# Performance work log

Measured on AMD Instinct MI355X. Metric: run time of the kernel, lower is better.

The kernel has to match this reference:

```python
import jax, jax.numpy as jnp
import numpy as np

B, T, C, H = 4, 4096, 1024, 64

def setup_inputs() -> dict:
    key = jax.random.key(0)
    k1, k2, k3, k4, k5 = jax.random.split(key, 5)
    scale = 0.02
    return {
        "x": jax.random.normal(k1, (B, T, C), dtype=jnp.float32),
        "head_bias": jax.random.normal(k2, (T, T), dtype=jnp.float32) * 0.1,
        "w_k": jax.random.normal(k3, (C, H), dtype=jnp.float32) * scale,
        "w_q": jax.random.normal(k4, (C, H), dtype=jnp.float32) * scale,
        "w_v": jax.random.normal(k5, (C, H), dtype=jnp.float32) * scale,
    }

def reference(x, head_bias, w_k, w_q, w_v):
    # x: (B,T,C) ; projections: (B,T,H)
    k = jnp.einsum('btc,ch->bth', x, w_k)
    q = jnp.einsum('btc,ch->bth', x, w_q)
    v = jnp.einsum('btc,ch->bth', x, w_v)
    Tq = x.shape[1]
    # scores: (B,T,T) with RPE bias and causal mask
    scores = jnp.einsum('bqh,bkh->bqk', q, k) * (k.shape[-1] ** -0.5)
    scores = scores + head_bias[None, :, :]
    causal = jnp.tril(jnp.ones((Tq, Tq), dtype=bool))
    scores = jnp.where(causal[None, :, :], scores, -jnp.inf)
    weights = jax.nn.softmax(scores, axis=-1)
    out = jnp.einsum('bqk,bkh->bqh', weights, v)
    return out
```

## Files before the change

kernel.cpp:

```cpp
#include <hip/hip_runtime.h>
#include <hip/hip_bf16.h>


#define T_DIM 4096
#define C_DIM 1024
#define KT    64
#define CK    256

typedef __attribute__((ext_vector_type(8))) short s16x8;
typedef __attribute__((ext_vector_type(4))) float f32x4;
typedef __attribute__((ext_vector_type(2))) unsigned int u32x2;

__device__ __forceinline__ short f2bf(float f) {
    unsigned u = __builtin_bit_cast(unsigned, f);
    u += 0x7FFFu + ((u >> 16) & 1u);
    return (short)(u >> 16);
}
__device__ __forceinline__ unsigned pack2(float a, float b) {
    unsigned ua = __builtin_bit_cast(unsigned, a);
    unsigned ub = __builtin_bit_cast(unsigned, b);
    ua += 0x7FFFu + ((ua >> 16) & 1u);
    ub += 0x7FFFu + ((ub >> 16) & 1u);
    return __builtin_amdgcn_perm(ub, ua, 0x07060302u);
}
__device__ __forceinline__ float bf2f(short s) {
    unsigned u = ((unsigned)(unsigned short)s) << 16;
    return __builtin_bit_cast(float, u);
}
__device__ __forceinline__ int chunk_off(int qt32) {
    int g = qt32 >> 3, r = qt32 & 7;
    return qt32 + 4 * g * (g - 1) + r * g;
}

__global__ __launch_bounds__(256) void prep_frag(
    const float* __restrict__ wk, const float* __restrict__ wq,
    const float* __restrict__ wv, short* __restrict__ wfrag)
{
    int ksAll = blockIdx.x, mat = blockIdx.y;
    const float* w = (mat == 0) ? wk : ((mat == 1) ? wq : wv);
    float sc = (mat == 1) ? 0.125f : 1.0f;
    int nt = threadIdx.x >> 6, lane = threadIdx.x & 63;
    int quad = lane >> 4, l15 = lane & 15;
    int h = nt * 16 + l15;
    int cb = ksAll * 32 + quad * 8;
    s16x8 v;
    #pragma unroll
    for (int j = 0; j < 8; ++j) v[j] = f2bf(w[(cb + j) * 64 + h] * sc);
    *(s16x8*)&wfrag[((ksAll * 12 + mat * 4 + nt) * 64 + lane) * 8] = v;
}

__global__ __launch_bounds__(256, 3) void proj_part(
    const float* __restrict__ x, const short* __restrict__ wfrag,
    short* __restrict__ pp)
{
    int w = threadIdx.x >> 6, lane = threadIdx.x & 63;
    int l15 = lane & 15, quad = lane >> 4;
    int row0 = (blockIdx.x * 4 + w) * 16;
    int cq = blockIdx.y;

    f32x4 acc[12];
    #pragma unroll
    for (int i = 0; i < 12; ++i) acc[i] = (f32x4){0.f, 0.f, 0.f, 0.f};

    const float* xrow = x + (size_t)(row0 + l15) * C_DIM + cq * 256;

    #pragma unroll 1
    for (int ksi = 0; ksi < 8; ++ksi) {
        int ks = (ksi + blockIdx.x) & 7;
        int ksAll = cq * 8 + ks;
        const s16x8* fb = (const s16x8*)&wfrag[(size_t)(ksAll * 12 * 64 + lane) * 8];
        f32x4 x0 = *(const f32x4*)(xrow + ks * 32 + quad * 8);
        f32x4 x1 = *(const f32x4*)(xrow + ks * 32 + quad * 8 + 4);
        s16x8 af;
        unsigned p0 = pack2(x0[0], x0[1]), p1 = pack2(x0[2], x0[3]);
        unsigned p2 = pack2(x1[0], x1[1]), p3 = pack2(x1[2], x1[3]);
        af[0] = (short)p0; af[1] = (short)(p0 >> 16);
        af[2] = (short)p1; af[3] = (short)(p1 >> 16);
        af[4] = (short)p2; af[5] = (short)(p2 >> 16);
        af[6] = (short)p3; af[7] = (short)(p3 >> 16);
        #pragma unroll
        for (int f = 0; f < 12; ++f) {
            s16x8 bf = fb[f * 64];
            acc[f] = __builtin_amdgcn_mfma_f32_16x16x32_bf16(af, bf, acc[f], 0, 0, 0);
        }
    }
    short* base = pp + (size_t)cq * 16384 * 192;
    #pragma unroll
    for (int f = 0; f < 12; ++f) {
        int mat = f >> 2, nt = f & 3;
        #pragma unroll
        for (int r = 0; r < 4; ++r)
            base[(size_t)(row0 + quad * 4 + r) * 192 + mat * 64 + nt * 16 + l15] =
                f2bf(acc[f][r]);
    }
}

__global__ __launch_bounds__(256) void proj_combine(
    const short* __restrict__ pp, short* __restrict__ qb,
    short* __restrict__ kfrag, short* __restrict__ vfrag)
{
    int m0 = blockIdx.x * 64;
    int b = m0 >> 12, t0 = m0 & 4095;
    __shared__ short vt[64][72];
    #pragma unroll
    for (int o = 0; o < 6; ++o) {
        int oct = o * 256 + threadIdx.x;
        int row = oct / 24, c8 = (oct - row * 24) * 8;
        float s[8];
        #pragma unroll
        for (int j = 0; j < 8; ++j) s[j] = 0.f;
        #pragma unroll
        for (int cq = 0; cq < 4; ++cq) {
            s16x8 v = *(const s16x8*)&pp[((size_t)cq * 16384 + m0 + row) * 192 + c8];
            #pragma unroll
            for (int j = 0; j < 8; ++j) s[j] += bf2f(v[j]);
        }
        s16x8 r;
        #pragma unroll
        for (int j = 0; j < 4; ++j) {
            unsigned d = pack2(s[2 * j], s[2 * j + 1]);
            r[2 * j] = (short)d; r[2 * j + 1] = (short)(d >> 16);
        }
        int t = t0 + row;
        if (c8 < 64) {
            int quad = (c8 >> 3) & 3, ks = c8 >> 5;
            int lane = quad * 16 + (t & 15);
            *(s16x8*)&kfrag[(size_t)(((b * 256 + (t >> 4)) * 2 + ks) * 64 + lane) * 8] = r;
        } else if (c8 < 128) {
            *(s16x8*)&qb[(size_t)(m0 + row) * 64 + (c8 - 64)] = r;
        } else {
            #pragma unroll
            for (int j = 0; j < 8; ++j) vt[c8 - 128 + j][row] = r[j];
        }
    }
    __syncthreads();
    #pragma unroll
    for (int rep = 0; rep < 2; ++rep) {
        int id = rep * 256 + threadIdx.x;
        int lane = id & 63, nt = (id >> 6) & 3, kl = id >> 8;
        int l15 = lane & 15, quad = lane >> 4;
        s16x8 v = *(const s16x8*)&vt[nt * 16 + l15][kl * 32 + quad * 8];
        *(s16x8*)&vfrag[(size_t)(((b * 128 + (t0 >> 5) + kl) * 4 + nt) * 64 + lane) * 8] = v;
    }
}

__global__ __launch_bounds__(512, 4) void flash_part(
    const short* __restrict__ qb, const short* __restrict__ kfrag,
    const short* __restrict__ vfrag, const float* __restrict__ bias,
    short* __restrict__ po)
{
    int qt = blockIdx.x, c = blockIdx.y;
    if (c > (qt >> 3)) return;
    int q0 = qt * 32;
    int kstart = c * CK;
    int kend = min(kstart + CK, q0 + 32);

    __shared__ __align__(16) short plds[8][16][72];

    int w = threadIdx.x >> 6, lane = threadIdx.x & 63;
    int b = w & 3, sl = w >> 2;
    int l15 = lane & 15, quad = lane >> 4;
    int strip0 = q0 + sl * 16;

    const short* qrow = qb + (size_t)(b * T_DIM + strip0 + l15) * 64;
    s16x8 aq0 = *(const s16x8*)(qrow + quad * 8);
    s16x8 aq1 = *(const s16x8*)(qrow + 32 + quad * 8);

    float l_sum = 0.f;
    f32x4 accO[4];
    #pragma unroll
    for (int nt = 0; nt < 4; ++nt) accO[nt] = (f32x4){0.f, 0.f, 0.f, 0.f};

    const float* brow = bias + (size_t)(strip0 + l15) * T_DIM;
    const short* kfb = kfrag + (size_t)b * 256 * 2 * 512;
    const short* vfb = vfrag + (size_t)b * 128 * 4 * 512;

    #pragma unroll 1
    for (int k0 = kstart; k0 < kend; k0 += KT) {
        int kt16 = k0 >> 4, kt32 = k0 >> 5;
        s16x8 ak0[4], ak1[4];
        #pragma unroll
        for (int nt = 0; nt < 4; ++nt) {
            const short* kp = kfb + (size_t)((kt16 + nt) * 2) * 512 + lane * 8;
            ak0[nt] = *(const s16x8*)kp;
            ak1[nt] = *(const s16x8*)(kp + 512);
        }
        f32x4 vb[4];
        #pragma unroll
        for (int nt = 0; nt < 4; ++nt)
            vb[nt] = *(const f32x4*)&brow[k0 + nt * 16 + quad * 4];

        f32x4 accS[4];
        #pragma unroll
        for (int nt = 0; nt < 4; ++nt) {
            accS[nt] = (f32x4){0.f, 0.f, 0.f, 0.f};
            accS[nt] = __builtin_amdgcn_mfma_f32_16x16x32_bf16(ak0[nt], aq0, accS[nt], 0, 0, 0);
            accS[nt] = __builtin_amdgcn_mfma_f32_16x16x32_bf16(ak1[nt], aq1, accS[nt], 0, 0, 0);
        }

        s16x8 bv0[4], bv1[4];
        #pragma unroll
        for (int nt = 0; nt < 4; ++nt) {
            const short* vp = vfb + (size_t)(kt32 * 4 + nt) * 512 + lane * 8;
            bv0[nt] = *(const s16x8*)vp;
            bv1[nt] = *(const s16x8*)(vp + 2048);
        }

        int qrow_g = strip0 + l15;
        bool diag = (k0 + KT - 1 > strip0);
        #pragma unroll
        for (int nt = 0; nt < 4; ++nt) {
            float sv[4];
            #pragma unroll
            for (int r = 0; r < 4; ++r) {
                sv[r] = accS[nt][r] + vb[nt][r];
                if (diag && (k0 + nt * 16 + quad * 4 + r > qrow_g))
                    sv[r] = -__builtin_inff();
                float p = __expf(sv[r]);
                sv[r] = p;
                l_sum += p;
            }
            u32x2 d;
            d[0] = pack2(sv[0], sv[1]);
            d[1] = pack2(sv[2], sv[3]);
            *(u32x2*)&plds[w][l15][nt * 16 + quad * 4] = d;
        }

        s16x8 ap0 = *(const s16x8*)&plds[w][l15][quad * 8];
        s16x8 ap1 = *(const s16x8*)&plds[w][l15][32 + quad * 8];
        #pragma unroll
        for (int nt = 0; nt < 4; ++nt) {
            accO[nt] = __builtin_amdgcn_mfma_f32_16x16x32_bf16(ap0, bv0[nt], accO[nt], 0, 0, 0);
            accO[nt] = __builtin_amdgcn_mfma_f32_16x16x32_bf16(ap1, bv1[nt], accO[nt], 0, 0, 0);
        }
    }

    l_sum += __shfl_xor(l_sum, 16, 64);
    l_sum += __shfl_xor(l_sum, 32, 64);

    short* base = po + (size_t)((chunk_off(qt) + c) * 4 + b) * 2080;
    #pragma unroll
    for (int nt = 0; nt < 4; ++nt)
        #pragma unroll
        for (int r = 0; r < 4; ++r)
            base[(sl * 16 + quad * 4 + r) * 64 + nt * 16 + l15] = f2bf(accO[nt][r]);
    if (quad == 0) base[2048 + sl * 16 + l15] = f2bf(l_sum);
}

__global__ __launch_bounds__(256) void flash_reduce(
    const short* __restrict__ po, float* __restrict__ out)
{
    int idx = blockIdx.x * 256 + threadIdx.x;
    int row = idx >> 4, c4 = idx & 15;
    int b = row >> 12, t = row & 4095;
    int qt = t >> 5, rloc = t & 31;
    int nc = (t >> 8) + 1;
    int off = chunk_off(qt);
    float o0 = 0.f, o1 = 0.f, o2 = 0.f, o3 = 0.f, l = 0.f;
    #pragma unroll 1
    for (int cc = 0; cc < nc; ++cc) {
        const short* base = po + (size_t)((off + cc) * 4 + b) * 2080;
        const short* p = &base[rloc * 64 + c4 * 4];
        o0 += bf2f(p[0]); o1 += bf2f(p[1]); o2 += bf2f(p[2]); o3 += bf2f(p[3]);
        l += bf2f(base[2048 + rloc]);
    }
    float inv = 1.0f / l;
    f32x4 res = (f32x4){o0 * inv, o1 * inv, o2 * inv, o3 * inv};
    *(f32x4*)&out[(size_t)row * 64 + c4 * 4] = res;
}

extern "C" void kernel_launch(void* const* d_in, const int* in_sizes, int n_in,
                              void* d_out, int out_size, void* d_ws, size_t ws_size,
                              hipStream_t stream) {
    (void)in_sizes; (void)n_in; (void)out_size; (void)ws_size;
    const float* x    = (const float*)d_in[0];
    const float* bias = (const float*)d_in[1];
    const float* wk   = (const float*)d_in[2];
    const float* wq   = (const float*)d_in[3];
    const float* wv   = (const float*)d_in[4];
    float* out = (float*)d_out;

    short* wfrag = (short*)d_ws;
    short* qb    = wfrag + 196608;
    short* kfrag = qb + 1048576;
    short* vfrag = kfrag + 1048576;
    short* pp    = vfrag + 1048576;
    short* po    = pp + (size_t)12582912;

    prep_frag<<<dim3(32, 3), dim3(256), 0, stream>>>(wk, wq, wv, wfrag);
    proj_part<<<dim3(256, 4), dim3(256), 0, stream>>>(x, wfrag, pp);
    proj_combine<<<dim3(256), dim3(256), 0, stream>>>(pp, qb, kfrag, vfrag);
    flash_part<<<dim3(128, 16), dim3(512), 0, stream>>>(qb, kfrag, vfrag, bias, po);
    flash_reduce<<<dim3(1024), dim3(256), 0, stream>>>(po, out);
}
```

Measured before the change: 229.3 us.

## Fuse projection split-K combine into one kernel and restructure flash tiling

The projection is now one kernel. Two wave groups each cover half of C and reduce through LDS, then write the Q/K/V fragment layouts directly, which removes the partial-product buffer and the separate combine launch. Flash attention now uses 16-row query tiles with 256-thread blocks and 32-key steps. K and bias loads are double-buffered to overlap memory with compute. The changes add more blocks and cheaper causal waste, but each block does less work and reuses K/V less.

```diff
diff --git a/kernel.cpp b/kernel.cpp
--- a/kernel.cpp
+++ b/kernel.cpp
@@ -4,7 +4,6 @@
 
 #define T_DIM 4096
 #define C_DIM 1024
-#define KT    64
 #define CK    256
 
 typedef __attribute__((ext_vector_type(8))) short s16x8;
@@ -27,9 +26,9 @@
     unsigned u = ((unsigned)(unsigned short)s) << 16;
     return __builtin_bit_cast(float, u);
 }
-__device__ __forceinline__ int chunk_off(int qt32) {
-    int g = qt32 >> 3, r = qt32 & 7;
-    return qt32 + 4 * g * (g - 1) + r * g;
+__device__ __forceinline__ int chunk_off(int qt) {
+    int g = qt >> 4, r = qt & 15;
+    return qt + 8 * g * (g - 1) + r * g;
 }
 
 __global__ __launch_bounds__(256) void prep_frag(
@@ -49,25 +48,29 @@
     *(s16x8*)&wfrag[((ksAll * 12 + mat * 4 + nt) * 64 + lane) * 8] = v;
 }
 
-__global__ __launch_bounds__(256, 3) void proj_part(
+__global__ __launch_bounds__(512, 2) void proj_fused(
     const float* __restrict__ x, const short* __restrict__ wfrag,
-    short* __restrict__ pp)
-{
-    int w = threadIdx.x >> 6, lane = threadIdx.x & 63;
+    short* __restrict__ qb, short* __restrict__ kfrag, short* __restrict__ vfrag)
+{
+    __shared__ __align__(16) short comb[4][16][136];
+    __shared__ __align__(16) short vsep[64][72];
+
+    int tid = threadIdx.x;
+    int w = tid >> 6, lane = tid & 63;
+    int g = w & 3, h = w >> 2;
     int l15 = lane & 15, quad = lane >> 4;
-    int row0 = (blockIdx.x * 4 + w) * 16;
-    int cq = blockIdx.y;
+    int m0 = blockIdx.x * 64;
+    int row0 = m0 + g * 16;
 
     f32x4 acc[12];
     #pragma unroll
     for (int i = 0; i < 12; ++i) acc[i] = (f32x4){0.f, 0.f, 0.f, 0.f};
 
-    const float* xrow = x + (size_t)(row0 + l15) * C_DIM + cq * 256;
+    const float* xrow = x + (size_t)(row0 + l15) * C_DIM + h * 512;
 
     #pragma unroll 1
-    for (int ksi = 0; ksi < 8; ++ksi) {
-        int ks = (ksi + blockIdx.x) & 7;
-        int ksAll = cq * 8 + ks;
+    for (int ks = 0; ks < 16; ++ks) {
+        int ksAll = h * 16 + ks;
         const s16x8* fb = (const s16x8*)&wfrag[(size_t)(ksAll * 12 * 64 + lane) * 8];
         f32x4 x0 = *(const f32x4*)(xrow + ks * 32 + quad * 8);
         f32x4 x1 = *(const f32x4*)(xrow + ks * 32 + quad * 8 + 4);
@@ -84,83 +87,122 @@
             acc[f] = __builtin_amdgcn_mfma_f32_16x16x32_bf16(af, bf, acc[f], 0, 0, 0);
         }
     }
-    short* base = pp + (size_t)cq * 16384 * 192;
-    #pragma unroll
-    for (int f = 0; f < 12; ++f) {
-        int mat = f >> 2, nt = f & 3;
-        #pragma unroll
-        for (int r = 0; r < 4; ++r)
-            base[(size_t)(row0 + quad * 4 + r) * 192 + mat * 64 + nt * 16 + l15] =
-                f2bf(acc[f][r]);
-    }
-}
-
-__global__ __launch_bounds__(256) void proj_combine(
-    const short* __restrict__ pp, short* __restrict__ qb,
-    short* __restrict__ kfrag, short* __restrict__ vfrag)
-{
-    int m0 = blockIdx.x * 64;
+
+    if (h == 1) {
+        #pragma unroll
+        for (int f = 0; f < 8; ++f)
+            #pragma unroll
+            for (int r = 0; r < 4; ++r)
+                comb[g][quad * 4 + r][(f >> 2) * 64 + (f & 3) * 16 + l15] = f2bf(acc[f][r]);
+        #pragma unroll
+        for (int f = 8; f < 12; ++f)
+            #pragma unroll
+            for (int r = 0; r < 4; ++r)
+                vsep[(f & 3) * 16 + l15][g * 16 + quad * 4 + r] = f2bf(acc[f][r]);
+    }
+    __syncthreads();
+    if (h == 0) {
+        #pragma unroll
+        for (int f = 0; f < 8; ++f)
+            #pragma unroll
+            for (int r = 0; r < 4; ++r) {
+                int col = (f >> 2) * 64 + (f & 3) * 16 + l15, rr = quad * 4 + r;
+                comb[g][rr][col] = f2bf(acc[f][r] + bf2f(comb[g][rr][col]));
+            }
+        #pragma unroll
+        for (int f = 8; f < 12; ++f)
+            #pragma unroll
+            for (int r = 0; r < 4; ++r) {
+                int hh = (f & 3) * 16 + l15, kk = g * 16 + quad * 4 + r;
+                vsep[hh][kk] = f2bf(acc[f][r] + bf2f(vsep[hh][kk]));
+            }
+    }
+    __syncthreads();
+
     int b = m0 >> 12, t0 = m0 & 4095;
-    __shared__ short vt[64][72];
-    #pragma unroll
-    for (int o = 0; o < 6; ++o) {
-        int oct = o * 256 + threadIdx.x;
-        int row = oct / 24, c8 = (oct - row * 24) * 8;
-        float s[8];
-        #pragma unroll
-        for (int j = 0; j < 8; ++j) s[j] = 0.f;
-        #pragma unroll
-        for (int cq = 0; cq < 4; ++cq) {
-            s16x8 v = *(const s16x8*)&pp[((size_t)cq * 16384 + m0 + row) * 192 + c8];
-            #pragma unroll
-            for (int j = 0; j < 8; ++j) s[j] += bf2f(v[j]);
-        }
-        s16x8 r;
-        #pragma unroll
-        for (int j = 0; j < 4; ++j) {
-            unsigned d = pack2(s[2 * j], s[2 * j + 1]);
-            r[2 * j] = (short)d; r[2 * j + 1] = (short)(d >> 16);
-        }
-        int t = t0 + row;
-        if (c8 < 64) {
-            int quad = (c8 >> 3) & 3, ks = c8 >> 5;
-            int lane = quad * 16 + (t & 15);
-            *(s16x8*)&kfrag[(size_t)(((b * 256 + (t >> 4)) * 2 + ks) * 64 + lane) * 8] = r;
-        } else if (c8 < 128) {
-            *(s16x8*)&qb[(size_t)(m0 + row) * 64 + (c8 - 64)] = r;
-        } else {
-            #pragma unroll
-            for (int j = 0; j < 8; ++j) vt[c8 - 128 + j][row] = r[j];
-        }
-    }
-    __syncthreads();
-    #pragma unroll
-    for (int rep = 0; rep < 2; ++rep) {
-        int id = rep * 256 + threadIdx.x;
-        int lane = id & 63, nt = (id >> 6) & 3, kl = id >> 8;
-        int l15 = lane & 15, quad = lane >> 4;
-        s16x8 v = *(const s16x8*)&vt[nt * 16 + l15][kl * 32 + quad * 8];
-        *(s16x8*)&vfrag[(size_t)(((b * 128 + (t0 >> 5) + kl) * 4 + nt) * 64 + lane) * 8] = v;
-    }
-}
-
-__global__ __launch_bounds__(512, 4) void flash_part(
+    {
+        int row = tid >> 3, ch = tid & 7;
+        s16x8 v = *(const s16x8*)&comb[row >> 4][row & 15][64 + ch * 8];
+        *(s16x8*)&qb[(size_t)(m0 + row) * 64 + ch * 8] = v;
+    }
+    {
+        int kt = w & 3, ks = w >> 2;
+        s16x8 v = *(const s16x8*)&comb[kt][l15][ks * 32 + quad * 8];
+        *(s16x8*)&kfrag[(size_t)(((b * 256 + (t0 >> 4) + kt) * 2 + ks) * 64 + lane) * 8] = v;
+    }
+    {
+        int kt32 = w & 1, nt = w >> 1;
+        s16x8 v = *(const s16x8*)&vsep[nt * 16 + l15][kt32 * 32 + quad * 8];
+        *(s16x8*)&vfrag[(size_t)(((b * 128 + (t0 >> 5) + kt32) * 4 + nt) * 64 + lane) * 8] = v;
+    }
+}
+
+#define LOADST(AK, VB, k0) do {                                               \
+    int _kt16 = (k0) >> 4;                                                    \
+    _Pragma("unroll")                                                         \
+    for (int _n = 0; _n < 2; ++_n) {                                          \
+        const short* _kp = kfb + (size_t)((_kt16 + _n) * 2) * 512 + lane * 8; \
+        AK[_n * 2]     = *(const s16x8*)_kp;                                  \
+        AK[_n * 2 + 1] = *(const s16x8*)(_kp + 512);                          \
+    }                                                                         \
+    _Pragma("unroll")                                                         \
+    for (int _n = 0; _n < 2; ++_n)                                            \
+        VB[_n] = *(const f32x4*)&brow[(k0) + _n * 16 + quad * 4];             \
+} while (0)
+
+#define COMPUTEST(AK, VB, k0) do {                                            \
+    int _kt32 = (k0) >> 5;                                                    \
+    s16x8 _bv[4];                                                             \
+    _Pragma("unroll")                                                         \
+    for (int _n = 0; _n < 4; ++_n)                                            \
+        _bv[_n] = *(const s16x8*)(vfb + (size_t)(_kt32 * 4 + _n) * 512 + lane * 8); \
+    f32x4 _aS[2];                                                             \
+    _Pragma("unroll")                                                         \
+    for (int _n = 0; _n < 2; ++_n) {                                          \
+        _aS[_n] = (f32x4){0.f, 0.f, 0.f, 0.f};                                \
+        _aS[_n] = __builtin_amdgcn_mfma_f32_16x16x32_bf16(AK[_n*2],   aq0, _aS[_n], 0, 0, 0); \
+        _aS[_n] = __builtin_amdgcn_mfma_f32_16x16x32_bf16(AK[_n*2+1], aq1, _aS[_n], 0, 0, 0); \
+    }                                                                         \
+    _Pragma("unroll")                                                         \
+    for (int _n = 0; _n < 2; ++_n) {                                          \
+        float _sv[4];                                                         \
+        _Pragma("unroll")                                                     \
+        for (int _r = 0; _r < 4; ++_r) {                                      \
+            _sv[_r] = _aS[_n][_r] + VB[_n][_r];                               \
+            if (mask_on && ((k0) + _n * 16 + quad * 4 + _r > strip0 + l15))   \
+                _sv[_r] = -__builtin_inff();                                  \
+            float _p = __expf(_sv[_r]);                                       \
+            _sv[_r] = _p;                                                     \
+            l_sum += _p;                                                      \
+        }                                                                     \
+        u32x2 _d;                                                             \
+        _d[0] = pack2(_sv[0], _sv[1]);                                        \
+        _d[1] = pack2(_sv[2], _sv[3]);                                        \
+        *(u32x2*)&plds[w][l15][_n * 16 + quad * 4] = _d;                      \
+    }                                                                         \
+    s16x8 _ap = *(const s16x8*)&plds[w][l15][quad * 8];                       \
+    _Pragma("unroll")                                                         \
+    for (int _n = 0; _n < 4; ++_n)                                            \
+        accO[_n] = __builtin_amdgcn_mfma_f32_16x16x32_bf16(_ap, _bv[_n], accO[_n], 0, 0, 0); \
+} while (0)
+
+__global__ __launch_bounds__(256, 4) void flash_part(
     const short* __restrict__ qb, const short* __restrict__ kfrag,
     const short* __restrict__ vfrag, const float* __restrict__ bias,
     short* __restrict__ po)
 {
     int qt = blockIdx.x, c = blockIdx.y;
-    if (c > (qt >> 3)) return;
-    int q0 = qt * 32;
+    if (c > (qt >> 4)) return;
+    int q0 = qt * 16;
     int kstart = c * CK;
-    int kend = min(kstart + CK, q0 + 32);
-
-    __shared__ __align__(16) short plds[8][16][72];
+    int kend = min(kstart + CK, q0 + 16);
+
+    __shared__ __align__(16) short plds[4][16][40];
 
     int w = threadIdx.x >> 6, lane = threadIdx.x & 63;
-    int b = w & 3, sl = w >> 2;
+    int b = w;
     int l15 = lane & 15, quad = lane >> 4;
-    int strip0 = q0 + sl * 16;
+    int strip0 = q0;
 
     const short* qrow = qb + (size_t)(b * T_DIM + strip0 + l15) * 64;
     s16x8 aq0 = *(const s16x8*)(qrow + quad * 8);
@@ -174,77 +216,36 @@
     const float* brow = bias + (size_t)(strip0 + l15) * T_DIM;
     const short* kfb = kfrag + (size_t)b * 256 * 2 * 512;
     const short* vfb = vfrag + (size_t)b * 128 * 4 * 512;
-
-    #pragma unroll 1
-    for (int k0 = kstart; k0 < kend; k0 += KT) {
-        int kt16 = k0 >> 4, kt32 = k0 >> 5;
-        s16x8 ak0[4], ak1[4];
-        #pragma unroll
-        for (int nt = 0; nt < 4; ++nt) {
-            const short* kp = kfb + (size_t)((kt16 + nt) * 2) * 512 + lane * 8;
-            ak0[nt] = *(const s16x8*)kp;
-            ak1[nt] = *(const s16x8*)(kp + 512);
-        }
-        f32x4 vb[4];
-        #pragma unroll
-        for (int nt = 0; nt < 4; ++nt)
-            vb[nt] = *(const f32x4*)&brow[k0 + nt * 16 + quad * 4];
-
-        f32x4 accS[4];
-        #pragma unroll
-        for (int nt = 0; nt < 4; ++nt) {
-            accS[nt] = (f32x4){0.f, 0.f, 0.f, 0.f};
-            accS[nt] = __builtin_amdgcn_mfma_f32_16x16x32_bf16(ak0[nt], aq0, accS[nt], 0, 0, 0);
-            accS[nt] = __builtin_amdgcn_mfma_f32_16x16x32_bf16(ak1[nt], aq1, accS[nt], 0, 0, 0);
-        }
-
-        s16x8 bv0[4], bv1[4];
-        #pragma unroll
-        for (int nt = 0; nt < 4; ++nt) {
-            const short* vp = vfb + (size_t)(kt32 * 4 + nt) * 512 + lane * 8;
-            bv0[nt] = *(const s16x8*)vp;
-            bv1[nt] = *(const s16x8*)(vp + 2048);
-        }
-
-        int qrow_g = strip0 + l15;
-        bool diag = (k0 + KT - 1 > strip0);
-        #pragma unroll
-        for (int nt = 0; nt < 4; ++nt) {
-            float sv[4];
-            #pragma unroll
-            for (int r = 0; r < 4; ++r) {
-                sv[r] = accS[nt][r] + vb[nt][r];
-                if (diag && (k0 + nt * 16 + quad * 4 + r > qrow_g))
-                    sv[r] = -__builtin_inff();
-                float p = __expf(sv[r]);
-                sv[r] = p;
-                l_sum += p;
-            }
-            u32x2 d;
-            d[0] = pack2(sv[0], sv[1]);
-            d[1] = pack2(sv[2], sv[3]);
-            *(u32x2*)&plds[w][l15][nt * 16 + quad * 4] = d;
-        }
-
-        s16x8 ap0 = *(const s16x8*)&plds[w][l15][quad * 8];
-        s16x8 ap1 = *(const s16x8*)&plds[w][l15][32 + quad * 8];
-        #pragma unroll
-        for (int nt = 0; nt < 4; ++nt) {
-            accO[nt] = __builtin_amdgcn_mfma_f32_16x16x32_bf16(ap0, bv0[nt], accO[nt], 0, 0, 0);
-            accO[nt] = __builtin_amdgcn_mfma_f32_16x16x32_bf16(ap1, bv1[nt], accO[nt], 0, 0, 0);
-        }
+    bool mask_on = (kend > strip0);
+
+    s16x8 akA[4], akB[4];
+    f32x4 vbA[2], vbB[2];
+    int k0 = kstart;
+    LOADST(akA, vbA, k0);
+    while (true) {
+        int k1 = k0 + 32;
+        bool more = (k1 < kend);
+        if (more) LOADST(akB, vbB, k1);
+        COMPUTEST(akA, vbA, k0);
+        if (!more) break;
+        k0 = k1; k1 = k0 + 32;
+        bool more2 = (k1 < kend);
+        if (more2) LOADST(akA, vbA, k1);
+        COMPUTEST(akB, vbB, k0);
+        if (!more2) break;
+        k0 = k1;
     }
 
     l_sum += __shfl_xor(l_sum, 16, 64);
     l_sum += __shfl_xor(l_sum, 32, 64);
 
-    short* base = po + (size_t)((chunk_off(qt) + c) * 4 + b) * 2080;
+    short* base = po + (size_t)((chunk_off(qt) + c) * 4 + b) * 1040;
     #pragma unroll
     for (int nt = 0; nt < 4; ++nt)
         #pragma unroll
         for (int r = 0; r < 4; ++r)
-            base[(sl * 16 + quad * 4 + r) * 64 + nt * 16 + l15] = f2bf(accO[nt][r]);
-    if (quad == 0) base[2048 + sl * 16 + l15] = f2bf(l_sum);
+            base[(quad * 4 + r) * 64 + nt * 16 + l15] = f2bf(accO[nt][r]);
+    if (quad == 0) base[1024 + l15] = f2bf(l_sum);
 }
 
 __global__ __launch_bounds__(256) void flash_reduce(
@@ -253,16 +254,16 @@
     int idx = blockIdx.x * 256 + threadIdx.x;
     int row = idx >> 4, c4 = idx & 15;
     int b = row >> 12, t = row & 4095;
-    int qt = t >> 5, rloc = t & 31;
+    int qt = t >> 4, rloc = t & 15;
     int nc = (t >> 8) + 1;
     int off = chunk_off(qt);
     float o0 = 0.f, o1 = 0.f, o2 = 0.f, o3 = 0.f, l = 0.f;
     #pragma unroll 1
     for (int cc = 0; cc < nc; ++cc) {
-        const short* base = po + (size_t)((off + cc) * 4 + b) * 2080;
+        const short* base = po + (size_t)((off + cc) * 4 + b) * 1040;
         const short* p = &base[rloc * 64 + c4 * 4];
         o0 += bf2f(p[0]); o1 += bf2f(p[1]); o2 += bf2f(p[2]); o3 += bf2f(p[3]);
-        l += bf2f(base[2048 + rloc]);
+        l += bf2f(base[1024 + rloc]);
     }
     float inv = 1.0f / l;
     f32x4 res = (f32x4){o0 * inv, o1 * inv, o2 * inv, o3 * inv};
@@ -284,12 +285,10 @@
     short* qb    = wfrag + 196608;
     short* kfrag = qb + 1048576;
     short* vfrag = kfrag + 1048576;
-    short* pp    = vfrag + 1048576;
-    short* po    = pp + (size_t)12582912;
+    short* po    = vfrag + 1048576;
 
     prep_frag<<<dim3(32, 3), dim3(256), 0, stream>>>(wk, wq, wv, wfrag);
-    proj_part<<<dim3(256, 4), dim3(256), 0, stream>>>(x, wfrag, pp);
-    proj_combine<<<dim3(256), dim3(256), 0, stream>>>(pp, qb, kfrag, vfrag);
-    flash_part<<<dim3(128, 16), dim3(512), 0, stream>>>(qb, kfrag, vfrag, bias, po);
+    proj_fused<<<dim3(256), dim3(512), 0, stream>>>(x, wfrag, qb, kfrag, vfrag);
+    flash_part<<<dim3(256, 16), dim3(256), 0, stream>>>(qb, kfrag, vfrag, bias, po);
     flash_reduce<<<dim3(1024), dim3(256), 0, stream>>>(po, out);
 }
```

After: 222.7 us. 1.03x faster.
